# Kernel optimization log

Hardware: AMD Instinct MI355X
Metric: run time of the kernel (lower is better)

The kernel has to match this reference:

```python
import jax, jax.numpy as jnp
import numpy as np

N_IN = 1024
N_OUT = 1024
L, B = 2048, 16


def setup_inputs() -> dict:
    key = jax.random.key(0)
    k1, k2 = jax.random.split(key, 2)
    val = (3.0 / N_IN) ** 0.5  # matches init_weight uniform range
    return {
        "x": jax.random.normal(k1, (L, B, N_IN), dtype=jnp.float32),
        "c0": jnp.zeros((B, N_OUT), dtype=jnp.float32),
        "weight": jax.random.uniform(k2, (N_IN, 3 * N_OUT), dtype=jnp.float32, minval=-val, maxval=val),
        "bias": jnp.zeros((2 * N_OUT,), dtype=jnp.float32),
    }


def reference(x, c0, weight, bias):
    # x: (L, B, n_in); weight: (n_in, 3*n_out); bias: (2*n_out,)
    Lx, Bx, _ = x.shape
    # u_ = x @ W, viewed as (L, B, n_out, k=3); bidir=1 dropped
    u = (x.reshape(Lx * Bx, N_IN) @ weight).reshape(Lx, Bx, N_OUT, 3)
    x_tilde = u[..., 0]                                  # (L, B, d)
    forget = jax.nn.sigmoid(u[..., 1] + bias[:N_OUT])    # (L, B, d)
    # sequential SRU recurrence: c_t = (c_{t-1} - x~_t) * f_t + x~_t
    def step(c_prev, inputs):
        xt, ft = inputs
        c = (c_prev - xt) * ft + xt
        return c, c
    c_final, cs = jax.lax.scan(step, c0, (x_tilde, forget))
    h = jnp.tanh(cs)  # activation_type == 1 (tanh); no highway, no dropout (eval)
    return h, c_final
```

## Files before the change

kernel.cpp:

```cpp
#include <hip/hip_runtime.h>


typedef __attribute__((ext_vector_type(8))) short short8;
typedef __attribute__((ext_vector_type(4))) float f32x4;

#define L_SEQ 2048
#define BATCH 16
#define NIN   1024
#define NOUT  1024
#define MROWS (L_SEQ * BATCH)
#define NCOLS (2 * NOUT)
#define ROWELEMS (BATCH * NOUT)
#define NCHUNK 32
#define CHLEN  64

__device__ __forceinline__ unsigned short f2bf(float f) {
  unsigned u = __float_as_uint(f);
  u += 0x7fffu + ((u >> 16) & 1u);
  return (unsigned short)(u >> 16);
}
__device__ __forceinline__ float bf2f(unsigned short b) {
  return __uint_as_float(((unsigned)b) << 16);
}
__device__ __forceinline__ float sigmoidf_(float x) {
  return __builtin_amdgcn_rcpf(1.f + __expf(-x));
}
__device__ __forceinline__ float fast_tanh(float x) {
  float ax = fabsf(x);
  float t = __expf(-2.f * ax);
  float r = (1.f - t) * __builtin_amdgcn_rcpf(1.f + t);
  return copysignf(r, x);
}

#define GLL16(gptr, lptr)                                              \
  __builtin_amdgcn_global_load_lds(                                    \
      (const __attribute__((address_space(1))) void*)(gptr),           \
      (__attribute__((address_space(3))) void*)(lptr), 16, 0, 0)

__global__ __launch_bounds__(256) void cvt_x_k(const float* __restrict__ x,
                                               unsigned short* __restrict__ o) {
  size_t i = ((size_t)blockIdx.x * 256 + threadIdx.x) * 8;
  const float4* p = (const float4*)(x + i);
  float4 a = p[0], b = p[1];
  union { unsigned short s[8]; uint4 v; } r;
  r.s[0] = f2bf(a.x); r.s[1] = f2bf(a.y); r.s[2] = f2bf(a.z); r.s[3] = f2bf(a.w);
  r.s[4] = f2bf(b.x); r.s[5] = f2bf(b.y); r.s[6] = f2bf(b.z); r.s[7] = f2bf(b.w);
  *(uint4*)(o + i) = r.v;
}

__global__ __launch_bounds__(256) void pack_w_k(const float* __restrict__ W,
                                                unsigned short* __restrict__ Bp) {
  int tid = blockIdx.x * 256 + threadIdx.x;
  int k = tid & (NIN - 1);
  int n = tid >> 10;
  int col = 3 * (n >> 1) + (n & 1);
  Bp[tid] = f2bf(W[(size_t)k * (3 * NOUT) + col]);
}

__global__ __launch_bounds__(256) void gemm_k(const unsigned short* __restrict__ A,
                                              const unsigned short* __restrict__ B,
                                              const float* __restrict__ bias,
                                              unsigned short* __restrict__ U) {
  __shared__ __align__(16) unsigned short As[128 * 32];
  __shared__ __align__(16) unsigned short Bs[128 * 32];
  const int K = NIN;
  int tid = threadIdx.x;
  int bi = blockIdx.x;
  int t = (bi & 7) * 512 + (bi >> 3);
  int n0 = (t & 15) << 7;
  int m0 = (t >> 4) << 7;
  int wave = tid >> 6;
  int lane = tid & 63;
  int wm = (wave >> 1) * 64;
  int wn = (wave & 1) * 64;
  int lr = lane & 15;
  int lk = (lane >> 4) * 8;

  f32x4 zero = {0.f, 0.f, 0.f, 0.f};
  f32x4 acc[4][4];
#pragma unroll
  for (int i = 0; i < 4; ++i)
#pragma unroll
    for (int j = 0; j < 4; ++j) acc[i][j] = zero;

  int srow = tid >> 2;
  int scol = (tid & 3) * 8;
  const unsigned short* gA = A + (size_t)(m0 + srow) * K + scol;
  const unsigned short* gB = B + (size_t)(n0 + srow) * K + scol;
  char* lA = (char*)As + (size_t)tid * 16;
  char* lB = (char*)Bs + (size_t)tid * 16;

  for (int kt = 0; kt < K; kt += 32) {
    GLL16(gA + kt, lA);
    GLL16(gA + (size_t)64 * K + kt, lA + 4096);
    GLL16(gB + kt, lB);
    GLL16(gB + (size_t)64 * K + kt, lB + 4096);
    __syncthreads();
    short8 af[4], bf_[4];
#pragma unroll
    for (int i = 0; i < 4; ++i)
      af[i] = *(const short8*)&As[(wm + i * 16 + lr) * 32 + lk];
#pragma unroll
    for (int j = 0; j < 4; ++j)
      bf_[j] = *(const short8*)&Bs[(wn + j * 16 + lr) * 32 + lk];
#pragma unroll
    for (int i = 0; i < 4; ++i)
#pragma unroll
      for (int j = 0; j < 4; ++j)
        acc[i][j] = __builtin_amdgcn_mfma_f32_16x16x32_bf16(af[i], bf_[j],
                                                            acc[i][j], 0, 0, 0);
    __syncthreads();
  }

  int mr = (lane >> 4) * 4;
  int nc = lane & 15;
#pragma unroll
  for (int i = 0; i < 4; ++i) {
#pragma unroll
    for (int j = 0; j < 4; ++j) {
      int n = n0 + wn + j * 16 + nc;
      float bsel = bias[n >> 1];
      bool isf = (n & 1);
#pragma unroll
      for (int r = 0; r < 4; ++r) {
        int m = m0 + wm + i * 16 + mr + r;
        float v = acc[i][j][r];
        if (isf) v = sigmoidf_(v + bsel);
        U[(size_t)m * NCOLS + n] = f2bf(v);
      }
    }
  }
}

__global__ __launch_bounds__(256) void scan_p1(const unsigned int* __restrict__ U2,
                                               float2* __restrict__ AV) {
  int tid = threadIdx.x;
  int bid = blockIdx.x;
  int bd = ((bid >> 7) << 10) + ((bid & 3) << 8) + tid;
  int chunk = (bid >> 2) & 31;
  const unsigned int* up = U2 + (size_t)chunk * CHLEN * ROWELEMS + bd;
  float a = 1.f, v = 0.f;
  for (int t0 = 0; t0 < CHLEN; t0 += 8) {
    unsigned int w[8];
#pragma unroll
    for (int j = 0; j < 8; ++j) w[j] = up[(size_t)(t0 + j) * ROWELEMS];
#pragma unroll
    for (int j = 0; j < 8; ++j) {
      float xt = bf2f((unsigned short)(w[j] & 0xffffu));
      float f  = bf2f((unsigned short)(w[j] >> 16));
      v = f * v + (1.f - f) * xt;
      a = a * f;
    }
  }
  AV[(size_t)chunk * ROWELEMS + bd] = make_float2(a, v);
}

__global__ __launch_bounds__(256) void scan_p2(const float2* __restrict__ AV,
                                               const float* __restrict__ c0,
                                               float* __restrict__ CS,
                                               float* __restrict__ out) {
  int bd = blockIdx.x * 256 + threadIdx.x;
  float c = c0[bd];
  float2 av[NCHUNK];
#pragma unroll
  for (int k = 0; k < NCHUNK; ++k) av[k] = AV[(size_t)k * ROWELEMS + bd];
#pragma unroll
  for (int k = 0; k < NCHUNK; ++k) {
    CS[(size_t)k * ROWELEMS + bd] = c;
    c = av[k].x * c + av[k].y;
  }
  out[(size_t)MROWS * NOUT + bd] = c;
}

__global__ __launch_bounds__(256) void scan_p3(const unsigned int* __restrict__ U2,
                                               const float* __restrict__ CS,
                                               float* __restrict__ out) {
  int tid = threadIdx.x;
  int bid = blockIdx.x;
  int bd = ((bid >> 7) << 10) + ((bid & 3) << 8) + tid;
  int chunk = (bid >> 2) & 31;
  float c = CS[(size_t)chunk * ROWELEMS + bd];
  const unsigned int* up = U2 + (size_t)chunk * CHLEN * ROWELEMS + bd;
  float* op = out + (size_t)chunk * CHLEN * ROWELEMS + bd;
  for (int t0 = 0; t0 < CHLEN; t0 += 8) {
    unsigned int w[8];
#pragma unroll
    for (int j = 0; j < 8; ++j) w[j] = up[(size_t)(t0 + j) * ROWELEMS];
#pragma unroll
    for (int j = 0; j < 8; ++j) {
      float xt = bf2f((unsigned short)(w[j] & 0xffffu));
      float f  = bf2f((unsigned short)(w[j] >> 16));
      c = (c - xt) * f + xt;
      op[(size_t)(t0 + j) * ROWELEMS] = fast_tanh(c);
    }
  }
}

extern "C" void kernel_launch(void* const* d_in, const int* in_sizes, int n_in,
                              void* d_out, int out_size, void* d_ws, size_t ws_size,
                              hipStream_t stream) {
  const float* x    = (const float*)d_in[0];
  const float* c0   = (const float*)d_in[1];
  const float* W    = (const float*)d_in[2];
  const float* bias = (const float*)d_in[3];
  float* out = (float*)d_out;

  char* ws = (char*)d_ws;
  unsigned short* Abf = (unsigned short*)ws;
  unsigned short* Bp  = (unsigned short*)(ws + ((size_t)64 << 20));
  unsigned short* U   = (unsigned short*)(ws + ((size_t)68 << 20));
  float2* AV = (float2*)ws;
  float*  CS = (float*)(ws + ((size_t)4 << 20));

  cvt_x_k<<<MROWS * NIN / (256 * 8), 256, 0, stream>>>(x, Abf);
  pack_w_k<<<NCOLS * NIN / 256, 256, 0, stream>>>(W, Bp);
  gemm_k<<<4096, 256, 0, stream>>>(Abf, Bp, bias, U);
  scan_p1<<<2048, 256, 0, stream>>>((const unsigned int*)U, AV);
  scan_p2<<<64, 256, 0, stream>>>(AV, c0, CS, out);
  scan_p3<<<2048, 256, 0, stream>>>((const unsigned int*)U, CS, out);
}
```

Baseline: 301.2 us.

## Rewrite GEMM as 256x256 tile, 8-wave double-buffered kernel with swizzled LDS

Replaces the 128x128 single-buffered bf16 MFMA GEMM with a 256x256-tile, 512-thread kernel. It uses K-steps of 64, double-buffered LDS loaded through global_load_lds, and an XOR swizzle to avoid bank conflicts. Global loads for the next K-step are interleaved with MFMA phases, ordered by barriers, setprio and vmcnt waits. The goal is to hide load latency and raise data reuse per tile, at the cost of 128KB of LDS and tricky manual synchronization.

```diff
diff --git a/kernel.cpp b/kernel.cpp
--- a/kernel.cpp
+++ b/kernel.cpp
@@ -13,6 +13,7 @@
 #define ROWELEMS (BATCH * NOUT)
 #define NCHUNK 32
 #define CHLEN  64
+#define NT 16
 
 __device__ __forceinline__ unsigned short f2bf(float f) {
   unsigned u = __float_as_uint(f);
@@ -57,79 +58,163 @@
   Bp[tid] = f2bf(W[(size_t)k * (3 * NOUT) + col]);
 }
 
-__global__ __launch_bounds__(256) void gemm_k(const unsigned short* __restrict__ A,
-                                              const unsigned short* __restrict__ B,
-                                              const float* __restrict__ bias,
-                                              unsigned short* __restrict__ U) {
-  __shared__ __align__(16) unsigned short As[128 * 32];
-  __shared__ __align__(16) unsigned short Bs[128 * 32];
+#define BARR __builtin_amdgcn_s_barrier()
+#define SCHED0 __builtin_amdgcn_sched_barrier(0)
+#define VMCNT(n) asm volatile("s_waitcnt vmcnt(" #n ")" ::: "memory")
+
+#define STAGE_A(bufc, ha, kt)                                                   \
+  do {                                                                          \
+    GLL16(pga##ha##0 + (kt) * 64, lds + (bufc) * 32768 + (ha) * 16384 + tid * 16);      \
+    GLL16(pga##ha##1 + (kt) * 64, lds + (bufc) * 32768 + (ha) * 16384 + 8192 + tid * 16); \
+  } while (0)
+#define STAGE_B(bufc, hb, kt)                                                   \
+  do {                                                                          \
+    GLL16(pgb##hb##0 + (kt) * 64, lds + 65536 + (bufc) * 32768 + (hb) * 16384 + tid * 16); \
+    GLL16(pgb##hb##1 + (kt) * 64, lds + 65536 + (bufc) * 32768 + (hb) * 16384 + 8192 + tid * 16); \
+  } while (0)
+
+#define LDA(DST, bufc, half)                                                    \
+  _Pragma("unroll") for (int i = 0; i < 4; ++i) {                               \
+    DST[i][0] = *(const short8*)(lds + (bufc) * 32768 + (half) * 16384 +        \
+                                 (rowAb + i * 16) * 128 + colX0);               \
+    DST[i][1] = *(const short8*)(lds + (bufc) * 32768 + (half) * 16384 +        \
+                                 (rowAb + i * 16) * 128 + colX1);               \
+  }
+#define LDB(DST, bufc, half)                                                    \
+  _Pragma("unroll") for (int j = 0; j < 2; ++j) {                               \
+    DST[j][0] = *(const short8*)(lds + 65536 + (bufc) * 32768 + (half) * 16384 + \
+                                 (rowBb + j * 16) * 128 + colX0);               \
+    DST[j][1] = *(const short8*)(lds + 65536 + (bufc) * 32768 + (half) * 16384 + \
+                                 (rowBb + j * 16) * 128 + colX1);               \
+  }
+
+#define MM(Q, AF, BF)                                                           \
+  _Pragma("unroll") for (int i = 0; i < 4; ++i)                                 \
+  _Pragma("unroll") for (int j = 0; j < 2; ++j) {                               \
+    Q[i][j] = __builtin_amdgcn_mfma_f32_16x16x32_bf16(AF[i][0], BF[j][0], Q[i][j], 0, 0, 0); \
+    Q[i][j] = __builtin_amdgcn_mfma_f32_16x16x32_bf16(AF[i][1], BF[j][1], Q[i][j], 0, 0, 0); \
+  }
+
+#define PH_TAIL(Q, AF, BF)                                                      \
+  BARR;                                                                         \
+  __builtin_amdgcn_s_setprio(1);                                                \
+  MM(Q, AF, BF);                                                                \
+  __builtin_amdgcn_s_setprio(0);                                                \
+  BARR;                                                                         \
+  SCHED0
+
+#define PH_TAILV(Q, AF, BF)                                                     \
+  BARR;                                                                         \
+  __builtin_amdgcn_s_setprio(1);                                                \
+  MM(Q, AF, BF);                                                                \
+  __builtin_amdgcn_s_setprio(0);                                                \
+  VMCNT(4);                                                                     \
+  BARR;                                                                         \
+  SCHED0
+
+#define EPI(Q, qm, qn)                                                          \
+  do {                                                                          \
+    _Pragma("unroll") for (int i = 0; i < 4; ++i)                               \
+    _Pragma("unroll") for (int j = 0; j < 2; ++j) {                             \
+      int n = n0 + (qn) * 128 + wn * 32 + j * 16 + nc;                          \
+      float bsel = bias[n >> 1];                                                \
+      _Pragma("unroll") for (int r = 0; r < 4; ++r) {                           \
+        int m = m0 + (qm) * 128 + wm * 64 + i * 16 + mr + r;                    \
+        float v = Q[i][j][r];                                                   \
+        if (isf) v = sigmoidf_(v + bsel);                                       \
+        U[(size_t)m * NCOLS + n] = f2bf(v);                                     \
+      }                                                                         \
+    }                                                                           \
+  } while (0)
+
+__global__ __launch_bounds__(512, 2) void gemm8_k(const unsigned short* __restrict__ A,
+                                                  const unsigned short* __restrict__ B,
+                                                  const float* __restrict__ bias,
+                                                  unsigned short* __restrict__ U) {
+  __shared__ __align__(16) char lds[131072];
   const int K = NIN;
   int tid = threadIdx.x;
-  int bi = blockIdx.x;
-  int t = (bi & 7) * 512 + (bi >> 3);
-  int n0 = (t & 15) << 7;
-  int m0 = (t >> 4) << 7;
   int wave = tid >> 6;
   int lane = tid & 63;
-  int wm = (wave >> 1) * 64;
-  int wn = (wave & 1) * 64;
+  int wm = wave >> 2;
+  int wn = wave & 3;
   int lr = lane & 15;
-  int lk = (lane >> 4) * 8;
+  int hi = lane >> 4;
+
+  int bi = blockIdx.x;
+  int t = (bi & 7) * 128 + (bi >> 3);
+  int n0 = (t & 7) << 8;
+  int m0 = (t >> 3) << 8;
+
+  int rowAb = wm * 64 + lr;
+  int rowBb = wn * 32 + lr;
+  int swz = (lr & 7) << 4;
+  int colX0 = (hi * 16) ^ swz;
+  int colX1 = (64 + hi * 16) ^ swz;
+
+  int row0 = tid >> 3;
+  int gch = (tid & 7) ^ (row0 & 7);
+  const unsigned short* pga00 = A + (size_t)(m0 + row0) * K + gch * 8;
+  const unsigned short* pga01 = pga00 + (size_t)64 * K;
+  const unsigned short* pga10 = pga00 + (size_t)128 * K;
+  const unsigned short* pga11 = pga00 + (size_t)192 * K;
+  const unsigned short* pgb00 = B + (size_t)(n0 + row0) * K + gch * 8;
+  const unsigned short* pgb01 = pgb00 + (size_t)64 * K;
+  const unsigned short* pgb10 = pgb00 + (size_t)128 * K;
+  const unsigned short* pgb11 = pgb00 + (size_t)192 * K;
 
   f32x4 zero = {0.f, 0.f, 0.f, 0.f};
-  f32x4 acc[4][4];
+  f32x4 acc00[4][2], acc01[4][2], acc11[4][2], acc10[4][2];
 #pragma unroll
   for (int i = 0; i < 4; ++i)
 #pragma unroll
-    for (int j = 0; j < 4; ++j) acc[i][j] = zero;
-
-  int srow = tid >> 2;
-  int scol = (tid & 3) * 8;
-  const unsigned short* gA = A + (size_t)(m0 + srow) * K + scol;
-  const unsigned short* gB = B + (size_t)(n0 + srow) * K + scol;
-  char* lA = (char*)As + (size_t)tid * 16;
-  char* lB = (char*)Bs + (size_t)tid * 16;
-
-  for (int kt = 0; kt < K; kt += 32) {
-    GLL16(gA + kt, lA);
-    GLL16(gA + (size_t)64 * K + kt, lA + 4096);
-    GLL16(gB + kt, lB);
-    GLL16(gB + (size_t)64 * K + kt, lB + 4096);
-    __syncthreads();
-    short8 af[4], bf_[4];
-#pragma unroll
-    for (int i = 0; i < 4; ++i)
-      af[i] = *(const short8*)&As[(wm + i * 16 + lr) * 32 + lk];
-#pragma unroll
-    for (int j = 0; j < 4; ++j)
-      bf_[j] = *(const short8*)&Bs[(wn + j * 16 + lr) * 32 + lk];
-#pragma unroll
-    for (int i = 0; i < 4; ++i)
-#pragma unroll
-      for (int j = 0; j < 4; ++j)
-        acc[i][j] = __builtin_amdgcn_mfma_f32_16x16x32_bf16(af[i], bf_[j],
-                                                            acc[i][j], 0, 0, 0);
-    __syncthreads();
-  }
-
-  int mr = (lane >> 4) * 4;
+    for (int j = 0; j < 2; ++j) {
+      acc00[i][j] = zero; acc01[i][j] = zero;
+      acc11[i][j] = zero; acc10[i][j] = zero;
+    }
+
+  short8 af[4][2], bq0[2][2], bq1[2][2];
+
+  STAGE_A(0, 0, 0); STAGE_A(0, 1, 0); STAGE_B(0, 0, 0); STAGE_B(0, 1, 0);
+  STAGE_A(1, 0, 1); STAGE_B(1, 1, 1);
+  VMCNT(4);
+  BARR;
+  SCHED0;
+
+  for (int it = 0; it < NT / 2; ++it) {
+    int kt = it * 2;
+    int k1 = kt + 1, k2 = (kt + 2) & (NT - 1), k3 = (kt + 3) & (NT - 1);
+    STAGE_B(1, 0, k1); STAGE_A(1, 1, k1);
+    LDA(af, 0, 0); LDB(bq0, 0, 0);
+    PH_TAIL(acc00, af, bq0);
+    LDB(bq1, 0, 1);
+    PH_TAIL(acc01, af, bq1);
+    STAGE_A(0, 0, k2);
+    LDA(af, 0, 1);
+    PH_TAIL(acc11, af, bq1);
+    STAGE_B(0, 1, k2);
+    PH_TAILV(acc10, af, bq0);
+    STAGE_A(0, 1, k2);
+    LDA(af, 1, 0); LDB(bq0, 1, 0);
+    PH_TAIL(acc00, af, bq0);
+    STAGE_B(0, 0, k2);
+    LDB(bq1, 1, 1);
+    PH_TAIL(acc01, af, bq1);
+    STAGE_A(1, 0, k3);
+    LDA(af, 1, 1);
+    PH_TAIL(acc11, af, bq1);
+    STAGE_B(1, 1, k3);
+    PH_TAILV(acc10, af, bq0);
+  }
+  VMCNT(0);
+
+  int mr = hi * 4;
   int nc = lane & 15;
-#pragma unroll
-  for (int i = 0; i < 4; ++i) {
-#pragma unroll
-    for (int j = 0; j < 4; ++j) {
-      int n = n0 + wn + j * 16 + nc;
-      float bsel = bias[n >> 1];
-      bool isf = (n & 1);
-#pragma unroll
-      for (int r = 0; r < 4; ++r) {
-        int m = m0 + wm + i * 16 + mr + r;
-        float v = acc[i][j][r];
-        if (isf) v = sigmoidf_(v + bsel);
-        U[(size_t)m * NCOLS + n] = f2bf(v);
-      }
-    }
-  }
+  bool isf = nc & 1;
+  EPI(acc00, 0, 0);
+  EPI(acc01, 0, 1);
+  EPI(acc11, 1, 1);
+  EPI(acc10, 1, 0);
 }
 
 __global__ __launch_bounds__(256) void scan_p1(const unsigned int* __restrict__ U2,
@@ -214,7 +299,7 @@
 
   cvt_x_k<<<MROWS * NIN / (256 * 8), 256, 0, stream>>>(x, Abf);
   pack_w_k<<<NCOLS * NIN / 256, 256, 0, stream>>>(W, Bp);
-  gemm_k<<<4096, 256, 0, stream>>>(Abf, Bp, bias, U);
+  gemm8_k<<<1024, 512, 0, stream>>>(Abf, Bp, bias, U);
   scan_p1<<<2048, 256, 0, stream>>>((const unsigned int*)U, AV);
   scan_p2<<<64, 256, 0, stream>>>(AV, c0, CS, out);
   scan_p3<<<2048, 256, 0, stream>>>((const unsigned int*)U, CS, out);
```

Result: faster. 257.6 us (-14.5%).
